# Optimization experiments

Measured on AMD Instinct MI355X. Metric: run time of the kernel, lower is better.

The kernel has to match this reference:

```python
import jax, jax.numpy as jnp
import numpy as np

LAYER_SHAPES = [(256, 64, 56, 56), (256, 128, 28, 28), (256, 256, 14, 14), (256, 512, 7, 7)]
NUM_REF = 2000


def _lid_layer(ref, q, k):
    """MLE LID estimate (Ma et al.) per query row.
    ref: [R, C] reference activations; q: [B, C] pooled query activations.
    """
    # Euclidean cdist via the expansion ||q||^2 - 2 q.ref^T + ||ref||^2
    d2 = (jnp.sum(q * q, axis=1, keepdims=True)
          - 2.0 * (q @ ref.T)
          + jnp.sum(ref * ref, axis=1)[None, :])            # [B, R]
    d = jnp.sqrt(jnp.maximum(d2, 0.0))
    # smallest k+1 distances, drop the nearest (mirrors sorted[:,1:k+1])
    neg_topk = jax.lax.top_k(-d, k + 1)[0]                   # descending in -d => ascending d
    dk = -neg_topk[:, 1:k + 1]                               # [B, k], ascending
    # LID = -k / sum_i log(d_i / d_k)
    return -k / jnp.sum(jnp.log(dk / dk[:, -1:]), axis=1)    # [B]


def setup_inputs() -> dict:
    key = jax.random.key(0)
    ks = jax.random.split(key, 12)
    inp = {}
    for i, shp in enumerate(LAYER_SHAPES):
        inp[f"feat{i}"] = jax.random.normal(ks[i], shp, dtype=jnp.float32)
        inp[f"ref{i}"] = jax.random.normal(ks[4 + i], (NUM_REF, shp[1]), dtype=jnp.float32)
    inp["reg_w"] = jax.random.normal(ks[8], (1, 4), dtype=jnp.float32)
    inp["reg_b"] = jax.random.normal(ks[9], (1,), dtype=jnp.float32)
    inp["k"] = 20
    return inp


def reference(feat0, feat1, feat2, feat3, ref0, ref1, ref2, ref3, reg_w, reg_b, k):
    feats = [feat0, feat1, feat2, feat3]
    refs = [ref0, ref1, ref2, ref3]
    lid_scores = []
    for f, r in zip(feats, refs):
        fq = jnp.mean(f.reshape(f.shape[0], f.shape[1], -1), axis=2)  # [B, C]
        lid_scores.append(_lid_layer(r, fq, k))
    lid_feat = jnp.stack(lid_scores, axis=1)                 # [B, num_layers]
    logit = lid_feat @ reg_w.T + reg_b                        # [B, 1]
    return jax.nn.sigmoid(logit)[:, 0]
```

## Files before the change

### kernel.cpp

```cpp
#include <hip/hip_runtime.h>
#include <cmath>

#define WS_FQ_OFF      0u
#define WS_R2_OFF      245760u
#define WS_LID_OFF     253760u
#define WS_G_OFF       262144u
#define G_LAYER_STRIDE 512000u
#define NREF           2000

#define POOL_BLOCKS 61440
__global__ __launch_bounds__(256) void pool_r2_kernel(const float* __restrict__ f0,
                                                      const float* __restrict__ f1,
                                                      const float* __restrict__ f2,
                                                      const float* __restrict__ f3,
                                                      const float* __restrict__ r0,
                                                      const float* __restrict__ r1,
                                                      const float* __restrict__ r2p,
                                                      const float* __restrict__ r3,
                                                      float* __restrict__ fq_all,
                                                      float* __restrict__ r2_all) {
    int blk = blockIdx.x;
    int w = threadIdx.x >> 6, lane = threadIdx.x & 63;

    if (blk < POOL_BLOCKS) {
        const float* feat; int HW; int fqo; int lblk;
        if (blk < 4096)        { feat = f0; HW = 3136; fqo = 0;      lblk = blk;         }
        else if (blk < 12288)  { feat = f1; HW = 784;  fqo = 16384;  lblk = blk - 4096;  }
        else if (blk < 28672)  { feat = f2; HW = 196;  fqo = 49152;  lblk = blk - 12288; }
        else                   { feat = f3; HW = 49;   fqo = 114688; lblk = blk - 28672; }
        size_t row = (size_t)lblk * 4 + w;
        const float* p = feat + row * (size_t)HW;
        float s = 0.f;
        if ((HW & 3) == 0) {
            const float4* p4 = (const float4*)p;
            int n4 = HW >> 2;
            for (int i = lane; i < n4; i += 64) {
                float4 v = p4[i];
                s += (v.x + v.y) + (v.z + v.w);
            }
        } else {
            for (int i = lane; i < HW; i += 64) s += p[i];
        }
        #pragma unroll
        for (int off = 32; off; off >>= 1) s += __shfl_down(s, off, 64);
        if (lane == 0) fq_all[fqo + row] = s * (1.0f / (float)HW);
    } else {
        int rb = blk - POOL_BLOCKS;
        int layer = rb / 500;
        int r = (rb % 500) * 4 + w;
        if (r >= NREF) return;
        const float* rp; int C;
        switch (layer) {
            case 0:  rp = r0;  C = 64;  break;
            case 1:  rp = r1;  C = 128; break;
            case 2:  rp = r2p; C = 256; break;
            default: rp = r3;  C = 512; break;
        }
        const float4* rowp = (const float4*)(rp + (size_t)r * C);
        int n4 = C >> 2;
        float s = 0.f;
        for (int i = lane; i < n4; i += 64) {
            float4 v = rowp[i];
            s += v.x*v.x + v.y*v.y + v.z*v.z + v.w*v.w;
        }
        #pragma unroll
        for (int off = 32; off; off >>= 1) s += __shfl_down(s, off, 64);
        if (lane == 0) r2_all[layer * NREF + r] = s;
    }
}

#define BM 64
#define BN 64
#define BK 32
#define LDT 68
__global__ __launch_bounds__(256) void gemm_all(const float* __restrict__ fq_all,
                                                const float* __restrict__ ref0,
                                                const float* __restrict__ ref1,
                                                const float* __restrict__ ref2,
                                                const float* __restrict__ ref3,
                                                float* __restrict__ G) {
    __shared__ __align__(16) float As[BK * LDT];
    __shared__ __align__(16) float Bs[BK * LDT];
    int layer = blockIdx.z;
    const float* B; int K;
    switch (layer) {
        case 0:  B = ref0; K = 64;  break;
        case 1:  B = ref1; K = 128; break;
        case 2:  B = ref2; K = 256; break;
        default: B = ref3; K = 512; break;
    }
    const int fqo[4] = {0, 16384, 49152, 114688};
    const float* A = fq_all + fqo[layer];
    float* Gout = G + (size_t)layer * G_LAYER_STRIDE;

    int t = threadIdx.x;
    int tq = t & 15, tr = t >> 4;
    int m0 = blockIdx.x * BM;
    int n0 = blockIdx.y * BN;
    int row0 = t >> 3;
    int kc4  = t & 7;
    float acc[4][4] = {};

    for (int k0 = 0; k0 < K; k0 += BK) {
        #pragma unroll
        for (int half = 0; half < 2; ++half) {
            int row = row0 + half * 32;
            float4 av = *(const float4*)(A + (size_t)(m0 + row) * K + k0 + kc4 * 4);
            int brow = n0 + row;
            float4 bv = make_float4(0.f, 0.f, 0.f, 0.f);
            if (brow < NREF) bv = *(const float4*)(B + (size_t)brow * K + k0 + kc4 * 4);
            As[(kc4*4 + 0) * LDT + row] = av.x;
            As[(kc4*4 + 1) * LDT + row] = av.y;
            As[(kc4*4 + 2) * LDT + row] = av.z;
            As[(kc4*4 + 3) * LDT + row] = av.w;
            Bs[(kc4*4 + 0) * LDT + row] = bv.x;
            Bs[(kc4*4 + 1) * LDT + row] = bv.y;
            Bs[(kc4*4 + 2) * LDT + row] = bv.z;
            Bs[(kc4*4 + 3) * LDT + row] = bv.w;
        }
        __syncthreads();
        #pragma unroll
        for (int kk = 0; kk < BK; ++kk) {
            float4 a = *(const float4*)&As[kk * LDT + tq * 4];
            float4 b = *(const float4*)&Bs[kk * LDT + tr * 4];
            acc[0][0] += a.x*b.x; acc[0][1] += a.x*b.y; acc[0][2] += a.x*b.z; acc[0][3] += a.x*b.w;
            acc[1][0] += a.y*b.x; acc[1][1] += a.y*b.y; acc[1][2] += a.y*b.z; acc[1][3] += a.y*b.w;
            acc[2][0] += a.z*b.x; acc[2][1] += a.z*b.y; acc[2][2] += a.z*b.z; acc[2][3] += a.z*b.w;
            acc[3][0] += a.w*b.x; acc[3][1] += a.w*b.y; acc[3][2] += a.w*b.z; acc[3][3] += a.w*b.w;
        }
        __syncthreads();
    }

    int rbase = n0 + tr * 4;
    if (rbase < NREF) {
        #pragma unroll
        for (int i = 0; i < 4; ++i) {
            float4 o = make_float4(acc[i][0], acc[i][1], acc[i][2], acc[i][3]);
            *(float4*)(Gout + (size_t)(m0 + tq*4 + i) * NREF + rbase) = o;
        }
    }
}

__global__ __launch_bounds__(256) void topk_lid_kernel(const float* __restrict__ fq_all,
                                                       const float* __restrict__ G_all,
                                                       const float* __restrict__ r2_all,
                                                       float* __restrict__ lid,
                                                       const int* __restrict__ kptr) {
    __shared__ __align__(16) float d2s[NREF];
    __shared__ unsigned hist[2048];
    __shared__ float redq[4], redm[4], redl[4];
    __shared__ unsigned long long red8[4];
    __shared__ int sh_B, sh_cbelow, sh_cnt;
    __shared__ float sh_dmin;

    const int Cs[4]   = {64, 128, 256, 512};
    const int fqo[4]  = {0, 16384, 49152, 114688};

    int b = blockIdx.x, layer = blockIdx.y;
    int t = threadIdx.x;
    int lane = t & 63, w = t >> 6;
    int k = kptr[0];
    if (k + 1 > NREF) k = NREF - 1;
    unsigned K1 = (unsigned)(k + 1);
    int C = Cs[layer];
    const float* fq = fq_all + fqo[layer] + (size_t)b * C;
    const float* Gb = G_all + (size_t)layer * G_LAYER_STRIDE + (size_t)b * NREF;
    const float* r2 = r2_all + layer * NREF;
    const float INF = __uint_as_float(0x7f800000u);

    for (int i = t; i < 2048; i += 256) hist[i] = 0u;
    if (t == 0) sh_cnt = 0;
    float s = 0.f;
    for (int c = t; c < C; c += 256) { float v = fq[c]; s += v * v; }
    #pragma unroll
    for (int off = 32; off; off >>= 1) s += __shfl_down(s, off, 64);
    if (lane == 0) redq[w] = s;
    __syncthreads();
    float q2 = redq[0] + redq[1] + redq[2] + redq[3];

    float minv = INF;
    for (int i = t; i < NREF / 4; i += 256) {
        float4 g = *(const float4*)(Gb + i * 4);
        float4 rr = *(const float4*)(r2 + i * 4);
        float d0 = q2 - 2.f * g.x + rr.x; d0 = d0 > 0.f ? d0 : 0.f;
        float d1 = q2 - 2.f * g.y + rr.y; d1 = d1 > 0.f ? d1 : 0.f;
        float d2_ = q2 - 2.f * g.z + rr.z; d2_ = d2_ > 0.f ? d2_ : 0.f;
        float d3 = q2 - 2.f * g.w + rr.w; d3 = d3 > 0.f ? d3 : 0.f;
        *(float4*)(d2s + i * 4) = make_float4(d0, d1, d2_, d3);
        atomicAdd(&hist[__float_as_uint(d0) >> 20], 1u);
        atomicAdd(&hist[__float_as_uint(d1) >> 20], 1u);
        atomicAdd(&hist[__float_as_uint(d2_) >> 20], 1u);
        atomicAdd(&hist[__float_as_uint(d3) >> 20], 1u);
        minv = fminf(minv, fminf(fminf(d0, d1), fminf(d2_, d3)));
    }
    #pragma unroll
    for (int off = 32; off; off >>= 1) minv = fminf(minv, __shfl_down(minv, off, 64));
    if (lane == 0) redm[w] = minv;
    __syncthreads();

    if (t < 64) {
        unsigned p = 0;
        int base = t * 32;
        #pragma unroll 4
        for (int i = 0; i < 32; ++i) p += hist[base + i];
        unsigned cum = p;
        #pragma unroll
        for (int off = 1; off < 64; off <<= 1) {
            unsigned o = __shfl_up(cum, off, 64);
            if (t >= off) cum += o;
        }
        unsigned excl = cum - p;
        if (excl < K1 && K1 <= cum) {
            unsigned run = excl;
            int binB = base;
            for (int i = 0; i < 32; ++i) {
                unsigned c = hist[base + i];
                if (run + c >= K1) { binB = base + i; break; }
                run += c;
            }
            sh_B = binB;
            sh_cbelow = (int)run;
        }
        if (t == 0) sh_dmin = fminf(fminf(redm[0], redm[1]), fminf(redm[2], redm[3]));
    }
    __syncthreads();

    int B = sh_B;
    float* cand = (float*)hist;
    float lsum = 0.f;
    for (int i = t; i < NREF; i += 256) {
        float v = d2s[i];
        int bin = (int)(__float_as_uint(v) >> 20);
        if (bin < B) {
            lsum += logf(v);
        } else if (bin == B) {
            int pos = atomicAdd(&sh_cnt, 1);
            cand[pos] = v;
        }
    }
    #pragma unroll
    for (int off = 32; off; off >>= 1) lsum += __shfl_down(lsum, off, 64);
    if (lane == 0) redl[w] = lsum;
    __syncthreads();

    int cnt = sh_cnt;
    int m = (int)K1 - sh_cbelow;
    if (cnt <= 64) {
        if (t < 64) {
            float mv = (t < cnt) ? cand[t] : INF;
            float csum = 0.f, dk = 0.f;
            for (int it = 0; it < m; ++it) {
                float x = mv;
                #pragma unroll
                for (int off = 32; off; off >>= 1) x = fminf(x, __shfl_xor(x, off, 64));
                csum += logf(x);
                dk = x;
                unsigned long long ball = __ballot(mv == x);
                int src = __ffsll(ball) - 1;
                if (t == src) mv = INF;
            }
            if (t == 0) {
                float lsum_tot = redl[0] + redl[1] + redl[2] + redl[3];
                float denom = 0.5f * (lsum_tot + csum - logf(sh_dmin) - (float)k * logf(dk));
                lid[b * 4 + layer] = -(float)k / denom;
            }
        }
    } else {
        float csum = 0.f, dk = 0.f;
        for (int it = 0; it < m; ++it) {
            unsigned long long best = ~0ull;
            for (int i = t; i < cnt; i += 256) {
                unsigned long long key =
                    ((unsigned long long)__float_as_uint(cand[i]) << 32) | (unsigned)i;
                if (key < best) best = key;
            }
            #pragma unroll
            for (int off = 32; off; off >>= 1) {
                unsigned long long o = __shfl_down(best, off, 64);
                if (o < best) best = o;
            }
            if (lane == 0) red8[w] = best;
            __syncthreads();
            unsigned long long mm = red8[0];
            #pragma unroll
            for (int ww = 1; ww < 4; ++ww) if (red8[ww] < mm) mm = red8[ww];
            float v = __uint_as_float((unsigned)(mm >> 32));
            if (t == 0) {
                csum += logf(v);
                dk = v;
                cand[(int)(mm & 0xffffffffu)] = INF;
            }
            __syncthreads();
        }
        if (t == 0) {
            float lsum_tot = redl[0] + redl[1] + redl[2] + redl[3];
            float denom = 0.5f * (lsum_tot + csum - logf(sh_dmin) - (float)k * logf(dk));
            lid[b * 4 + layer] = -(float)k / denom;
        }
    }
}

__global__ __launch_bounds__(256) void head_kernel(const float* __restrict__ lid,
                                                   const float* __restrict__ w,
                                                   const float* __restrict__ bias,
                                                   float* __restrict__ out) {
    int b = threadIdx.x;
    float acc = bias[0];
    #pragma unroll
    for (int l = 0; l < 4; ++l) acc += lid[b * 4 + l] * w[l];
    out[b] = 1.f / (1.f + expf(-acc));
}

extern "C" void kernel_launch(void* const* d_in, const int* in_sizes, int n_in,
                              void* d_out, int out_size, void* d_ws, size_t ws_size,
                              hipStream_t stream) {
    const float* feat[4] = {(const float*)d_in[0], (const float*)d_in[2],
                            (const float*)d_in[4], (const float*)d_in[6]};
    const float* ref[4]  = {(const float*)d_in[1], (const float*)d_in[3],
                            (const float*)d_in[5], (const float*)d_in[7]};
    const float* reg_w = (const float*)d_in[8];
    const float* reg_b = (const float*)d_in[9];
    const int*   kptr  = (const int*)d_in[10];

    float* ws     = (float*)d_ws;
    float* fq_all = ws + WS_FQ_OFF;
    float* r2_all = ws + WS_R2_OFF;
    float* lid    = ws + WS_LID_OFF;
    float* G      = ws + WS_G_OFF;

    pool_r2_kernel<<<POOL_BLOCKS + 2000, 256, 0, stream>>>(
        feat[0], feat[1], feat[2], feat[3],
        ref[0], ref[1], ref[2], ref[3],
        fq_all, r2_all);

    gemm_all<<<dim3(256 / BM, (NREF + BN - 1) / BN, 4), 256, 0, stream>>>(
        fq_all, ref[0], ref[1], ref[2], ref[3], G);

    topk_lid_kernel<<<dim3(256, 4), 256, 0, stream>>>(fq_all, G, r2_all, lid, kptr);

    head_kernel<<<1, 256, 0, stream>>>(lid, reg_w, reg_b, (float*)d_out);
}
```

Measured before the change: 472.6 us.

## Stage fixed-size feature chunks in LDS for uniform coalesced pooling

The pooling kernel now gives every block the same 12544-float contiguous chunk of a feature tensor. Each chunk is loaded into shared memory with fully coalesced float4 loads, then per-row sums are computed from LDS with a mapping chosen for each layer's HW. This replaces the old one-wave-per-row scheme, which launched 61440 blocks and did poorly aligned scalar loads for HW=196 and HW=49. The ref-norm blocks now loop over all four layers per row, and the launch shrinks to 8180 blocks; the cost is about 50KB of LDS per block, which caps occupancy.

```diff
diff --git a/kernel.cpp b/kernel.cpp
--- a/kernel.cpp
+++ b/kernel.cpp
@@ -8,7 +8,6 @@
 #define G_LAYER_STRIDE 512000u
 #define NREF           2000
 
-#define POOL_BLOCKS 61440
 __global__ __launch_bounds__(256) void pool_r2_kernel(const float* __restrict__ f0,
                                                       const float* __restrict__ f1,
                                                       const float* __restrict__ f2,
@@ -19,53 +18,94 @@
                                                       const float* __restrict__ r3,
                                                       float* __restrict__ fq_all,
                                                       float* __restrict__ r2_all) {
+    __shared__ __align__(16) float tile[12544];
     int blk = blockIdx.x;
-    int w = threadIdx.x >> 6, lane = threadIdx.x & 63;
-
-    if (blk < POOL_BLOCKS) {
-        const float* feat; int HW; int fqo; int lblk;
-        if (blk < 4096)        { feat = f0; HW = 3136; fqo = 0;      lblk = blk;         }
-        else if (blk < 12288)  { feat = f1; HW = 784;  fqo = 16384;  lblk = blk - 4096;  }
-        else if (blk < 28672)  { feat = f2; HW = 196;  fqo = 49152;  lblk = blk - 12288; }
-        else                   { feat = f3; HW = 49;   fqo = 114688; lblk = blk - 28672; }
-        size_t row = (size_t)lblk * 4 + w;
-        const float* p = feat + row * (size_t)HW;
-        float s = 0.f;
-        if ((HW & 3) == 0) {
-            const float4* p4 = (const float4*)p;
-            int n4 = HW >> 2;
-            for (int i = lane; i < n4; i += 64) {
-                float4 v = p4[i];
-                s += (v.x + v.y) + (v.z + v.w);
-            }
+    int t = threadIdx.x;
+    int w = t >> 6, lane = t & 63;
+
+    if (blk < 7680) {
+        const float* src; float inv; int fqbase; int rows0;
+        if (blk < 4096)      { src = f0 + (size_t)blk * 12544;          inv = 1.0f/3136.f; fqbase = 0;      rows0 = blk * 4;            }
+        else if (blk < 6144) { src = f1 + (size_t)(blk - 4096) * 12544; inv = 1.0f/784.f;  fqbase = 16384;  rows0 = (blk - 4096) * 16;  }
+        else if (blk < 7168) { src = f2 + (size_t)(blk - 6144) * 12544; inv = 1.0f/196.f;  fqbase = 49152;  rows0 = (blk - 6144) * 64;  }
+        else                 { src = f3 + (size_t)(blk - 7168) * 12544; inv = 1.0f/49.f;   fqbase = 114688; rows0 = (blk - 7168) * 256; }
+
+        {
+            const float4* g4 = (const float4*)src;
+            float4* l4 = (float4*)tile;
+            float4 v[12];
+            #pragma unroll
+            for (int j = 0; j < 12; ++j) v[j] = g4[t + j * 256];
+            float4 vt;
+            if (t < 64) vt = g4[3072 + t];
+            #pragma unroll
+            for (int j = 0; j < 12; ++j) l4[t + j * 256] = v[j];
+            if (t < 64) l4[3072 + t] = vt;
+        }
+        __syncthreads();
+
+        if (blk < 4096) {
+            const float* rp = tile + w * 3136;
+            float s = 0.f;
+            #pragma unroll
+            for (int j = 0; j < 49; ++j) s += rp[j * 64 + lane];
+            #pragma unroll
+            for (int off = 32; off; off >>= 1) s += __shfl_down(s, off, 64);
+            if (lane == 0) fq_all[rows0 + w] = s * inv;
+        } else if (blk < 6144) {
+            int row = t >> 4, p = t & 15;
+            const float* rp = tile + row * 784 + p * 49;
+            float s = 0.f;
+            #pragma unroll
+            for (int j = 0; j < 49; ++j) s += rp[j];
+            s += __shfl_xor(s, 8, 64);
+            s += __shfl_xor(s, 4, 64);
+            s += __shfl_xor(s, 2, 64);
+            s += __shfl_xor(s, 1, 64);
+            if (p == 0) fq_all[fqbase + rows0 + row] = s * inv;
+        } else if (blk < 7168) {
+            int row = t >> 2, p = t & 3;
+            const float* rp = tile + row * 196 + p * 49;
+            float s = 0.f;
+            #pragma unroll
+            for (int j = 0; j < 49; ++j) s += rp[j];
+            s += __shfl_xor(s, 2, 64);
+            s += __shfl_xor(s, 1, 64);
+            if (p == 0) fq_all[fqbase + rows0 + row] = s * inv;
         } else {
-            for (int i = lane; i < HW; i += 64) s += p[i];
-        }
-        #pragma unroll
-        for (int off = 32; off; off >>= 1) s += __shfl_down(s, off, 64);
-        if (lane == 0) fq_all[fqo + row] = s * (1.0f / (float)HW);
+            const float* rp = tile + t * 49;
+            float s = 0.f;
+            #pragma unroll
+            for (int j = 0; j < 49; ++j) s += rp[j];
+            fq_all[fqbase + rows0 + t] = s * inv;
+        }
     } else {
-        int rb = blk - POOL_BLOCKS;
-        int layer = rb / 500;
-        int r = (rb % 500) * 4 + w;
-        if (r >= NREF) return;
-        const float* rp; int C;
-        switch (layer) {
-            case 0:  rp = r0;  C = 64;  break;
-            case 1:  rp = r1;  C = 128; break;
-            case 2:  rp = r2p; C = 256; break;
-            default: rp = r3;  C = 512; break;
-        }
-        const float4* rowp = (const float4*)(rp + (size_t)r * C);
-        int n4 = C >> 2;
-        float s = 0.f;
-        for (int i = lane; i < n4; i += 64) {
-            float4 v = rowp[i];
-            s += v.x*v.x + v.y*v.y + v.z*v.z + v.w*v.w;
-        }
-        #pragma unroll
-        for (int off = 32; off; off >>= 1) s += __shfl_down(s, off, 64);
-        if (lane == 0) r2_all[layer * NREF + r] = s;
+        int r4 = (blk - 7680) * 4 + w;
+        int layer = r4 >> 9;
+        (void)layer;
+        int r = r4;
+        if (r < NREF) {
+            #pragma unroll 1
+            for (int l = 0; l < 4; ++l) {
+                const float* rp; int C;
+                switch (l) {
+                    case 0:  rp = r0;  C = 64;  break;
+                    case 1:  rp = r1;  C = 128; break;
+                    case 2:  rp = r2p; C = 256; break;
+                    default: rp = r3;  C = 512; break;
+                }
+                const float4* rowp = (const float4*)(rp + (size_t)r * C);
+                int n4 = C >> 2;
+                float s = 0.f;
+                for (int i = lane; i < n4; i += 64) {
+                    float4 v = rowp[i];
+                    s += v.x*v.x + v.y*v.y + v.z*v.z + v.w*v.w;
+                }
+                #pragma unroll
+                for (int off = 32; off; off >>= 1) s += __shfl_down(s, off, 64);
+                if (lane == 0) r2_all[l * NREF + r] = s;
+            }
+        }
     }
 }
 
@@ -328,7 +368,7 @@
     float* lid    = ws + WS_LID_OFF;
     float* G      = ws + WS_G_OFF;
 
-    pool_r2_kernel<<<POOL_BLOCKS + 2000, 256, 0, stream>>>(
+    pool_r2_kernel<<<8180, 256, 0, stream>>>(
         feat[0], feat[1], feat[2], feat[3],
         ref[0], ref[1], ref[2], ref[3],
         fq_all, r2_all);
```

After: 454.7 us. 3.8% less time.
